# Performance work log

Measured on AMD Instinct MI355X. Metric: run time of the kernel, lower is better.

Reference implementation:

```python
import jax, jax.numpy as jnp
import numpy as np

EPS = 1e-6
HH = 4  # nheads


def _ln(x, g, b):
    mu = jnp.mean(x, axis=-1, keepdims=True)
    var = jnp.mean((x - mu) ** 2, axis=-1, keepdims=True)
    return (x - mu) * jax.lax.rsqrt(var + 1e-5) * g + b


def setup_inputs() -> dict:
    key = jax.random.key(0)
    ks = jax.random.split(key, 12)
    B, T, C, H, W = 4, 32, 128, 32, 32
    Gd = 64
    s_in = 1.0 / np.sqrt(C + Gd)
    s_c = 1.0 / np.sqrt(C)
    s_f = 1.0 / np.sqrt(4 * C)
    return {
        "x": jax.random.normal(ks[0], (B, T, C, H, W), jnp.float32),
        "guidance": jax.random.normal(ks[1], (B, T, Gd), jnp.float32),
        "Wq": jax.random.uniform(ks[2], (C + Gd, C), jnp.float32, -s_in, s_in),
        "bq": jnp.zeros((C,), jnp.float32),
        "Wk": jax.random.uniform(ks[3], (C + Gd, C), jnp.float32, -s_in, s_in),
        "bk": jnp.zeros((C,), jnp.float32),
        "Wv": jax.random.uniform(ks[4], (C, C), jnp.float32, -s_c, s_c),
        "bv": jnp.zeros((C,), jnp.float32),
        "ln1_g": jnp.ones((C,), jnp.float32),
        "ln1_b": jnp.zeros((C,), jnp.float32),
        "ln2_g": jnp.ones((C,), jnp.float32),
        "ln2_b": jnp.zeros((C,), jnp.float32),
        "W1": jax.random.uniform(ks[5], (C, 4 * C), jnp.float32, -s_c, s_c),
        "b1": jnp.zeros((4 * C,), jnp.float32),
        "W2": jax.random.uniform(ks[6], (4 * C, C), jnp.float32, -s_f, s_f),
        "b2": jnp.zeros((C,), jnp.float32),
    }


def reference(x, guidance, Wq, bq, Wk, bk, Wv, bv, ln1_g, ln1_b, ln2_g, ln2_b, W1, b1, W2, b2):
    B, T, C, H, W = x.shape
    Gd = guidance.shape[-1]
    N = B * H * W
    Hd = C // HH
    # (B,T,C,H,W) -> (N,T,C)
    x_bhw = jnp.transpose(x, (0, 3, 4, 1, 2)).reshape(N, T, C)
    g = jnp.broadcast_to(guidance[:, None, None, :, :], (B, H, W, T, Gd)).reshape(N, T, Gd)
    xqk = jnp.concatenate([x_bhw, g], axis=-1)
    q = (xqk @ Wq + bq).reshape(N, T, HH, Hd)
    k = (xqk @ Wk + bk).reshape(N, T, HH, Hd)
    v = (x_bhw @ Wv + bv).reshape(N, T, HH, Hd)
    # elu feature-map linear attention (eval mode, dropout off)
    Q = jax.nn.elu(q) + 1.0
    K = jax.nn.elu(k) + 1.0
    Vn = v / T
    KV = jnp.einsum('nshd,nshv->nhdv', K, Vn)
    Z = 1.0 / (jnp.einsum('nlhd,nhd->nlh', Q, K.sum(axis=1)) + EPS)
    out = jnp.einsum('nlhd,nhdv->nlhv', Q, KV) * Z[..., None] * T
    out = out.reshape(N, T, C)
    out = out + _ln(x_bhw, ln1_g, ln1_b)
    h = _ln(out, ln2_g, ln2_b)
    h = jax.nn.gelu(h @ W1 + b1, approximate=False) @ W2 + b2
    out = out + h
    return jnp.transpose(out.reshape(B, H, W, T, C), (0, 3, 4, 1, 2))
```

## Files before the change

kernel.cpp:

```cpp
#include <hip/hip_runtime.h>
#include <hip/hip_bf16.h>
#include <math.h>

#define T_   32
#define C_   128
#define GD_  64
#define KQK_ 192
#define NH_  4
#define HD_  32
#define C4_  512
#define HW_  1024

typedef unsigned short u16;
typedef __attribute__((ext_vector_type(8))) short short8;
typedef __attribute__((ext_vector_type(4))) short short4v;
typedef __attribute__((ext_vector_type(4))) float f32x4;
typedef __attribute__((ext_vector_type(4))) unsigned short u16x4;

#define ACF_A 0
#define ACF_C 512
#define WQH 2048
#define WQL 26624
#define WKH 51200
#define WKL 75776
#define WVH 100352
#define WVL 116736
#define W1H 133120
#define W1L 198656
#define W2H 264192
#define W2L 329728
#define GSH 395264
#define GSL 403456
#define XT  411648
#define WS_NEED_BYTES (823296ull + 4096ull*8192ull*2ull)

#define AX_H  0
#define AX_L  25600
#define X2G(g) ((g)*8704)
#define HM_H  34816
#define HM_L  52224
#define KSUM  69632
#define ZDEN  70656
#define STATS 71680
#define LN2P  72704
#define POOLB 74752

__device__ __forceinline__ float b2f(u16 u) {
    unsigned int x = ((unsigned int)u) << 16;
    float f; __builtin_memcpy(&f, &x, 4); return f;
}
__device__ __forceinline__ u16 f2b(float f) {
    __hip_bfloat16 h = __float2bfloat16(f);
    u16 u; __builtin_memcpy(&u, &h, 2); return u;
}
__device__ __forceinline__ void split2(float v, u16& h, u16& l) {
    h = f2b(v); l = f2b(v - b2f(h));
}
__device__ __forceinline__ void splitfrag(const f32x4 v, short4v& h, short4v& l) {
    u16 hh[4], ll[4];
    #pragma unroll
    for (int r = 0; r < 4; ++r) { hh[r] = f2b(v[r]); ll[r] = f2b(v[r] - b2f(hh[r])); }
    h = (short4v){(short)hh[0],(short)hh[1],(short)hh[2],(short)hh[3]};
    l = (short4v){(short)ll[0],(short)ll[1],(short)ll[2],(short)ll[3]};
}

__device__ __forceinline__ f32x4 mfma16(short4v a, short4v b, f32x4 c) {
#if __has_builtin(__builtin_amdgcn_mfma_f32_16x16x16bf16_1k)
    return __builtin_amdgcn_mfma_f32_16x16x16bf16_1k(a, b, c, 0, 0, 0);
#else
    asm("v_mfma_f32_16x16x16_bf16 %0, %1, %2, %0" : "+v"(c) : "v"(a), "v"(b));
    return c;
#endif
}

#define MFMA3(acc, ah, al, bh, bl)                                          \
    acc = __builtin_amdgcn_mfma_f32_16x16x32_bf16(ah, bh, acc, 0, 0, 0);    \
    acc = __builtin_amdgcn_mfma_f32_16x16x32_bf16(ah, bl, acc, 0, 0, 0);    \
    acc = __builtin_amdgcn_mfma_f32_16x16x32_bf16(al, bh, acc, 0, 0, 0);

#define MFMA3_16(acc, ah, al, bh, bl)                                       \
    acc = mfma16(ah, bh, acc);                                              \
    acc = mfma16(ah, bl, acc);                                              \
    acc = mfma16(al, bh, acc);

__global__ void prep_weights(const float* __restrict__ Wq, const float* __restrict__ Wk,
                             const float* __restrict__ Wv, const float* __restrict__ W1,
                             const float* __restrict__ W2, const float* __restrict__ gui,
                             const float* __restrict__ g2, const float* __restrict__ be2,
                             const float* __restrict__ b1,
                             u16* __restrict__ wsp)
{
    int e = blockIdx.x * 256 + threadIdx.x;
    if (e >= 204800) {
        int n = e - 204800;
        if (n >= 512) return;
        float a = 0.f, c = 0.f;
        for (int k = 0; k < 128; ++k) {
            float w = W1[k*512 + n];
            a = fmaf(w, g2[k], a);
            c = fmaf(w, be2[k], c);
        }
        float* acf = (float*)wsp;
        acf[ACF_A + n] = a;
        acf[ACF_C + n] = c + b1[n];
        return;
    }
    if (e >= 196608) {
        int idx = e - 196608;
        float v = gui[idx];
        u16 hb = f2b(v);
        wsp[GSH + idx] = hb;
        wsp[GSL + idx] = f2b(v - b2f(hb));
        return;
    }
    const float* src; int e2, k, n, K; int oh, ol; int isW1 = 0;
    if (e < 24576)       { src = Wq; e2 = e;          k = e2 >> 7; n = e2 & 127; K = KQK_; oh = WQH; ol = WQL; }
    else if (e < 49152)  { src = Wk; e2 = e - 24576;  k = e2 >> 7; n = e2 & 127; K = KQK_; oh = WKH; ol = WKL; }
    else if (e < 65536)  { src = Wv; e2 = e - 49152;  k = e2 >> 7; n = e2 & 127; K = C_;   oh = WVH; ol = WVL; }
    else if (e < 131072) { src = W1; e2 = e - 65536;  k = e2 >> 9; n = e2 & 511; K = C_;   oh = W1H; ol = W1L; isW1 = 1; }
    else                 { src = W2; e2 = e - 131072; k = e2 >> 7; n = e2 & 127; K = C4_;  oh = W2H; ol = W2L; }
    float w = src[e2];
    if (isW1) w *= g2[k];
    u16 hb = f2b(w);
    wsp[oh + n * K + k] = hb;
    wsp[ol + n * K + k] = f2b(w - b2f(hb));
}

__global__ __launch_bounds__(256) void transpose_x(const float* __restrict__ x, u16* __restrict__ wsp)
{
    __shared__ float tile[32][65];
    int bid = blockIdx.x;
    int hq = bid & 15, cq = (bid >> 4) & 3, t = (bid >> 6) & 31, b = bid >> 11;
    int c0 = cq * 32, hw0 = hq * 64;
    int tid = threadIdx.x;
    {
        int i = tid >> 3, j8 = (tid & 7) * 8;
        const float* src = x + ((size_t)((b*32 + t)*128 + c0 + i))*1024 + hw0 + j8;
        float4 v0 = *reinterpret_cast<const float4*>(src);
        float4 v1 = *reinterpret_cast<const float4*>(src + 4);
        tile[i][j8+0]=v0.x; tile[i][j8+1]=v0.y; tile[i][j8+2]=v0.z; tile[i][j8+3]=v0.w;
        tile[i][j8+4]=v1.x; tile[i][j8+5]=v1.y; tile[i][j8+6]=v1.z; tile[i][j8+7]=v1.w;
    }
    __syncthreads();
    {
        int jj = tid >> 2, c8 = (tid & 3) * 8;
        int n = b*1024 + hw0 + jj;
        u16 hh[8], ll[8];
        #pragma unroll
        for (int ii = 0; ii < 8; ++ii) {
            float v = tile[c8 + ii][jj];
            u16 hb = f2b(v);
            hh[ii] = hb; ll[ii] = f2b(v - b2f(hb));
        }
        u16* dh = wsp + XT + (size_t)n*8192 + t*128 + c0 + c8;
        u16* dl = dh + 4096;
        *reinterpret_cast<ushort4*>(dh)     = make_ushort4(hh[0],hh[1],hh[2],hh[3]);
        *reinterpret_cast<ushort4*>(dh + 4) = make_ushort4(hh[4],hh[5],hh[6],hh[7]);
        *reinterpret_cast<ushort4*>(dl)     = make_ushort4(ll[0],ll[1],ll[2],ll[3]);
        *reinterpret_cast<ushort4*>(dl + 4) = make_ushort4(ll[4],ll[5],ll[6],ll[7]);
    }
}

__global__ __launch_bounds__(256, 2) void fused_linattn_mfma(
    const float* __restrict__ x,
    const float* __restrict__ bq, const float* __restrict__ bk, const float* __restrict__ bv,
    const float* __restrict__ g1, const float* __restrict__ be1,
    const float* __restrict__ b2,
    const u16* __restrict__ wsp, int use_xt,
    float* __restrict__ out)
{
    extern __shared__ __align__(16) char pool[];
    float* ksum  = (float*)(pool + KSUM);
    float* zf    = (float*)(pool + ZDEN);
    float* stats = (float*)(pool + STATS);
    float* ln2p  = (float*)(pool + LN2P);
    const float* acf = (const float*)wsp;

    const int bi  = blockIdx.x;
    const int j_  = ((bi & 7) << 8) | (bi >> 3);
    const int n0  = j_ * 2;
    const int b   = n0 >> 10;
    const int hw0 = n0 & 1023;
    const int tid = threadIdx.x;
    const int lane = tid & 63, wv = tid >> 6;
    const int l16  = lane & 15, quad = lane >> 4;

    short8 wqh[6][2], wql[6][2];
    #pragma unroll
    for (int ks = 0; ks < 6; ++ks)
        #pragma unroll
        for (int nt = 0; nt < 2; ++nt) {
            const int n = (wv*2 + nt)*16 + l16;
            wqh[ks][nt] = *(const short8*)(wsp + WQH + n*KQK_ + ks*32 + quad*8);
            wql[ks][nt] = *(const short8*)(wsp + WQL + n*KQK_ + ks*32 + quad*8);
        }

    if (use_xt) {
        #pragma unroll
        for (int tau = 0; tau < 2; ++tau) {
            const u16* xtb = wsp + XT + (size_t)(n0 + tau) * 8192;
            #pragma unroll
            for (int i = 0; i < 2; ++i) {
                int off = (tid + i*256) * 8;
                int t = off >> 7, c = off & 127;
                short8 vh = *reinterpret_cast<const short8*>(xtb + off);
                short8 vl = *reinterpret_cast<const short8*>(xtb + 4096 + off);
                *reinterpret_cast<short8*>(pool + AX_H + (tau*32 + t)*400 + c*2) = vh;
                *reinterpret_cast<short8*>(pool + AX_L + (tau*32 + t)*400 + c*2) = vl;
            }
        }
    } else {
        #pragma unroll
        for (int tau = 0; tau < 2; ++tau) {
            const float* xb = x + (size_t)b * (T_*C_*HW_) + hw0 + tau;
            #pragma unroll
            for (int i = 0; i < 16; ++i) {
                int idx = tid + i*256;
                float v = xb[(size_t)idx * HW_];
                int t = idx >> 7, c = idx & 127;
                u16 hb = f2b(v);
                *(u16*)(pool + AX_H + (tau*32 + t)*400 + c*2) = hb;
                *(u16*)(pool + AX_L + (tau*32 + t)*400 + c*2) = f2b(v - b2f(hb));
            }
        }
    }
    {
        const u16* gh = wsp + GSH + b*2048 + tid*8;
        const u16* gl = wsp + GSL + b*2048 + tid*8;
        int off = tid * 8;
        int t = off >> 6, jg = off & 63;
        short8 vh = *reinterpret_cast<const short8*>(gh);
        short8 vl = *reinterpret_cast<const short8*>(gl);
        *reinterpret_cast<short8*>(pool + AX_H + t*400 + 256 + jg*2) = vh;
        *reinterpret_cast<short8*>(pool + AX_L + t*400 + 256 + jg*2) = vl;
        *reinterpret_cast<short8*>(pool + AX_H + (32 + t)*400 + 256 + jg*2) = vh;
        *reinterpret_cast<short8*>(pool + AX_L + (32 + t)*400 + 256 + jg*2) = vl;
    }
    __syncthreads();

    short4v qfh[4][2], qfl[4][2];
    short4v kfh[4][2], kfl[4][2];
    short4v vfh[4][2], vfl[4][2];

    {
        f32x4 aq[4][2];
        #pragma unroll
        for (int mt = 0; mt < 4; ++mt)
            #pragma unroll
            for (int nt = 0; nt < 2; ++nt) aq[mt][nt] = (f32x4){0.f,0.f,0.f,0.f};
        #pragma unroll
        for (int ks = 0; ks < 6; ++ks) {
            short8 ah[4], al[4];
            #pragma unroll
            for (int mt = 0; mt < 4; ++mt) {
                ah[mt] = *(const short8*)(pool + AX_H + (mt*16 + l16)*400 + ks*64 + quad*16);
                al[mt] = *(const short8*)(pool + AX_L + (mt*16 + l16)*400 + ks*64 + quad*16);
            }
            #pragma unroll
            for (int nt = 0; nt < 2; ++nt)
                #pragma unroll
                for (int mt = 0; mt < 4; ++mt) { MFMA3(aq[mt][nt], wqh[ks][nt], wql[ks][nt], ah[mt], al[mt]); }
        }
        #pragma unroll
        for (int ct = 0; ct < 2; ++ct) {
            f32x4 bq4 = *(const f32x4*)(bq + wv*32 + ct*16 + quad*4);
            #pragma unroll
            for (int mt = 0; mt < 4; ++mt) {
                f32x4 qp;
                #pragma unroll
                for (int r = 0; r < 4; ++r) {
                    float q = aq[mt][ct][r] + bq4[r];
                    qp[r] = (q > 0.f) ? q + 1.f : __expf(q);
                }
                splitfrag(qp, qfh[mt][ct], qfl[mt][ct]);
            }
        }
    }

    {
        f32x4 ak[4][2];
        #pragma unroll
        for (int mt = 0; mt < 4; ++mt)
            #pragma unroll
            for (int nt = 0; nt < 2; ++nt) ak[mt][nt] = (f32x4){0.f,0.f,0.f,0.f};
        #pragma unroll
        for (int ks = 0; ks < 6; ++ks) {
            short8 ah[4], al[4];
            #pragma unroll
            for (int mt = 0; mt < 4; ++mt) {
                ah[mt] = *(const short8*)(pool + AX_H + (mt*16 + l16)*400 + ks*64 + quad*16);
                al[mt] = *(const short8*)(pool + AX_L + (mt*16 + l16)*400 + ks*64 + quad*16);
            }
            #pragma unroll
            for (int nt = 0; nt < 2; ++nt) {
                const int n = (wv*2 + nt)*16 + l16;
                short8 bh = *(const short8*)(wsp + WKH + n*KQK_ + ks*32 + quad*8);
                short8 bl = *(const short8*)(wsp + WKL + n*KQK_ + ks*32 + quad*8);
                #pragma unroll
                for (int mt = 0; mt < 4; ++mt) { MFMA3(ak[mt][nt], ah[mt], al[mt], bh, bl); }
            }
        }
        float sk[2][2] = {{0.f,0.f},{0.f,0.f}};
        #pragma unroll
        for (int nt = 0; nt < 2; ++nt) {
            float bias = bk[wv*32 + nt*16 + l16];
            #pragma unroll
            for (int mt = 0; mt < 4; ++mt) {
                f32x4 kp;
                #pragma unroll
                for (int r = 0; r < 4; ++r) {
                    float k = ak[mt][nt][r] + bias;
                    float v = (k > 0.f) ? k + 1.f : __expf(k);
                    kp[r] = v;
                    sk[mt >> 1][nt] += v;
                }
                splitfrag(kp, kfh[mt][nt], kfl[mt][nt]);
            }
        }
        #pragma unroll
        for (int tau = 0; tau < 2; ++tau)
            #pragma unroll
            for (int nt = 0; nt < 2; ++nt) {
                float s = sk[tau][nt];
                s += __shfl_xor(s, 16); s += __shfl_xor(s, 32);
                if (quad == 0) ksum[tau*128 + wv*32 + nt*16 + l16] = s;
            }
    }

    {
        f32x4 av[4][2];
        #pragma unroll
        for (int mt = 0; mt < 4; ++mt)
            #pragma unroll
            for (int nt = 0; nt < 2; ++nt) av[mt][nt] = (f32x4){0.f,0.f,0.f,0.f};
        #pragma unroll
        for (int ks = 0; ks < 4; ++ks) {
            short8 ah[4], al[4];
            #pragma unroll
            for (int mt = 0; mt < 4; ++mt) {
                ah[mt] = *(const short8*)(pool + AX_H + (mt*16 + l16)*400 + ks*64 + quad*16);
                al[mt] = *(const short8*)(pool + AX_L + (mt*16 + l16)*400 + ks*64 + quad*16);
            }
            #pragma unroll
            for (int nt = 0; nt < 2; ++nt) {
                const int n = (wv*2 + nt)*16 + l16;
                short8 bh = *(const short8*)(wsp + WVH + n*C_ + ks*32 + quad*8);
                short8 bl = *(const short8*)(wsp + WVL + n*C_ + ks*32 + quad*8);
                #pragma unroll
                for (int mt = 0; mt < 4; ++mt) { MFMA3(av[mt][nt], ah[mt], al[mt], bh, bl); }
            }
        }
        #pragma unroll
        for (int nt = 0; nt < 2; ++nt) {
            float bias = bv[wv*32 + nt*16 + l16];
            #pragma unroll
            for (int mt = 0; mt < 4; ++mt) {
                f32x4 vp;
                #pragma unroll
                for (int r = 0; r < 4; ++r) vp[r] = av[mt][nt][r] + bias;
                splitfrag(vp, vfh[mt][nt], vfl[mt][nt]);
            }
        }
    }

    #pragma unroll
    for (int tau = 0; tau < 2; ++tau) {
        f32x4 ka0 = *(const f32x4*)(ksum + tau*128 + wv*32 + quad*4);
        f32x4 ka1 = *(const f32x4*)(ksum + tau*128 + wv*32 + 16 + quad*4);
        #pragma unroll
        for (int lt = 0; lt < 2; ++lt) {
            const int mt = tau*2 + lt;
            float p = 0.f;
            #pragma unroll
            for (int i = 0; i < 4; ++i) {
                p = fmaf(b2f((u16)(short)qfh[mt][0][i]) + b2f((u16)(short)qfl[mt][0][i]), ka0[i], p);
                p = fmaf(b2f((u16)(short)qfh[mt][1][i]) + b2f((u16)(short)qfl[mt][1][i]), ka1[i], p);
            }
            p += __shfl_xor(p, 16); p += __shfl_xor(p, 32);
            if (quad == 0) zf[tau*128 + wv*32 + lt*16 + l16] = 1.f / (p + 1e-6f);
        }
    }

    short4v kvfh[2][2][2], kvfl[2][2][2];
    #pragma unroll
    for (int tau = 0; tau < 2; ++tau)
        #pragma unroll
        for (int dt = 0; dt < 2; ++dt)
            #pragma unroll
            for (int vt = 0; vt < 2; ++vt) {
                f32x4 kv = (f32x4){0.f,0.f,0.f,0.f};
                #pragma unroll
                for (int lt = 0; lt < 2; ++lt) {
                    const int mt = tau*2 + lt;
                    MFMA3_16(kv, kfh[mt][dt], kfl[mt][dt], vfh[mt][vt], vfl[mt][vt]);
                }
                splitfrag(kv, kvfh[tau][dt][vt], kvfl[tau][dt][vt]);
            }

    {
        int t = tid >> 2, jj = tid & 3;
        const char* rp = pool + AX_H + t*400 + jj*64;
        float m = 0.f, s = 0.f;
        #pragma unroll
        for (int p8 = 0; p8 < 4; ++p8) {
            short8 h = *(const short8*)(rp + p8*16);
            short8 l = *(const short8*)(rp + (AX_L - AX_H) + p8*16);
            #pragma unroll
            for (int i = 0; i < 8; ++i) {
                float v = b2f((u16)h[i]) + b2f((u16)l[i]);
                m += v; s = fmaf(v, v, s);
            }
        }
        m += __shfl_xor(m, 1); s += __shfl_xor(s, 1);
        m += __shfl_xor(m, 2); s += __shfl_xor(s, 2);
        if (jj == 0) {
            float mu = m * (1.f/C_);
            stats[t]      = mu;
            stats[64 + t] = rsqrtf(s * (1.f/C_) - mu*mu + 1e-5f);
        }
    }
    __syncthreads();

    f32x4 o1v[4][2];
    #pragma unroll
    for (int mt = 0; mt < 4; ++mt) {
        const int tau = mt >> 1;
        f32x4 zd4 = *(const f32x4*)(zf + tau*128 + wv*32 + (mt & 1)*16 + quad*4);
        f32x4 mu4 = *(const f32x4*)(stats + mt*16 + quad*4);
        f32x4 rs4 = *(const f32x4*)(stats + 64 + mt*16 + quad*4);
        #pragma unroll
        for (int vt = 0; vt < 2; ++vt) {
            f32x4 oa = (f32x4){0.f,0.f,0.f,0.f};
            #pragma unroll
            for (int dt = 0; dt < 2; ++dt) {
                MFMA3_16(oa, qfh[mt][dt], qfl[mt][dt], kvfh[tau][dt][vt], kvfl[tau][dt][vt]);
            }
            int ch = wv*32 + vt*16 + l16;
            float g1c = g1[ch], be1c = be1[ch];
            #pragma unroll
            for (int r = 0; r < 4; ++r) {
                int row = mt*16 + quad*4 + r;
                float xv = b2f(*(const u16*)(pool + AX_H + row*400 + ch*2))
                         + b2f(*(const u16*)(pool + AX_L + row*400 + ch*2));
                o1v[mt][vt][r] = oa[r]*zd4[r] + (xv - mu4[r])*rs4[r]*g1c + be1c;
            }
        }
    }
    {
        #pragma unroll
        for (int mt = 0; mt < 4; ++mt)
            #pragma unroll
            for (int r = 0; r < 4; ++r) {
                float v0 = o1v[mt][0][r], v1 = o1v[mt][1][r];
                float m = v0 + v1;
                float s = v0*v0 + v1*v1;
                m += __shfl_xor(m, 1); s += __shfl_xor(s, 1);
                m += __shfl_xor(m, 2); s += __shfl_xor(s, 2);
                m += __shfl_xor(m, 4); s += __shfl_xor(s, 4);
                m += __shfl_xor(m, 8); s += __shfl_xor(s, 8);
                if (l16 == 0) {
                    int row = mt*16 + quad*4 + r;
                    ln2p[wv*64 + row]       = m;
                    ln2p[256 + wv*64 + row] = s;
                }
            }
    }
    __syncthreads();

    #pragma unroll
    for (int mt = 0; mt < 4; ++mt) {
        char* xb = pool + X2G(mt);
        #pragma unroll
        for (int vt = 0; vt < 2; ++vt) {
            int ch = wv*32 + vt*16 + l16;
            #pragma unroll
            for (int r = 0; r < 4; ++r) {
                u16 hb, lb; split2(o1v[mt][vt][r], hb, lb);
                int off = (quad*4 + r)*272 + ch*2;
                *(u16*)(xb + off)        = hb;
                *(u16*)(xb + 4352 + off) = lb;
            }
        }
    }
    if (tid < 64) {
        int t = tid;
        float m = 0.f, s = 0.f;
        #pragma unroll
        for (int w = 0; w < 4; ++w) { m += ln2p[w*64 + t]; s += ln2p[256 + w*64 + t]; }
        float mu = m * (1.f/C_);
        float rs = rsqrtf(s * (1.f/C_) - mu*mu + 1e-5f);
        stats[128 + t] = mu * rs;
        stats[192 + t] = rs;
    }
    __syncthreads();

    f32x4 accO[4][2];
    #pragma unroll
    for (int mt = 0; mt < 4; ++mt)
        #pragma unroll
        for (int nt = 0; nt < 2; ++nt) accO[mt][nt] = (f32x4){0.f,0.f,0.f,0.f};

    #pragma unroll 1
    for (int mh = 0; mh < 4; ++mh) {
        {
            f32x4 accH[4][2];
            #pragma unroll
            for (int mt = 0; mt < 4; ++mt)
                #pragma unroll
                for (int nt = 0; nt < 2; ++nt) accH[mt][nt] = (f32x4){0.f,0.f,0.f,0.f};
            #pragma unroll
            for (int ks = 0; ks < 4; ++ks) {
                short8 ah[4], al[4];
                #pragma unroll
                for (int mt = 0; mt < 4; ++mt) {
                    const char* xb = pool + X2G(mt) + l16*272 + ks*64 + quad*16;
                    ah[mt] = *(const short8*)(xb);
                    al[mt] = *(const short8*)(xb + 4352);
                }
                #pragma unroll
                for (int nt = 0; nt < 2; ++nt) {
                    const int gn = mh*128 + (wv*2 + nt)*16 + l16;
                    short8 bh = *(const short8*)(wsp + W1H + gn*C_ + ks*32 + quad*8);
                    short8 bl = *(const short8*)(wsp + W1L + gn*C_ + ks*32 + quad*8);
                    #pragma unroll
                    for (int mt = 0; mt < 4; ++mt) { MFMA3(accH[mt][nt], bh, bl, ah[mt], al[mt]); }
                }
            }
            #pragma unroll
            for (int nt = 0; nt < 2; ++nt) {
                int base = mh*128 + (wv*2 + nt)*16 + quad*4;
                f32x4 a4 = *(const f32x4*)(acf + ACF_A + base);
                f32x4 c4 = *(const f32x4*)(acf + ACF_C + base);
                int ch0 = (wv*2 + nt)*16 + quad*4;
                #pragma unroll
                for (int mt = 0; mt < 4; ++mt) {
                    int tk = mt*16 + l16;
                    float mrs = stats[128 + tk], rsv = stats[192 + tk];
                    u16 hh[4], ll[4];
                    #pragma unroll
                    for (int r = 0; r < 4; ++r) {
                        float v = accH[mt][nt][r]*rsv - mrs*a4[r] + c4[r];
                        float ge = 0.5f * v * (1.f + erff(v * 0.70710678118654752f));
                        split2(ge, hh[r], ll[r]);
                    }
                    char* hb = pool + HM_H + tk*272 + ch0*2;
                    *(u16x4*)(hb)                    = (u16x4){hh[0],hh[1],hh[2],hh[3]};
                    *(u16x4*)(hb + (HM_L - HM_H))    = (u16x4){ll[0],ll[1],ll[2],ll[3]};
                }
            }
        }
        __syncthreads();
        {
            #pragma unroll
            for (int ks = 0; ks < 4; ++ks) {
                short8 ah[4], al[4];
                #pragma unroll
                for (int mt = 0; mt < 4; ++mt) {
                    const char* hb = pool + HM_H + (mt*16 + l16)*272 + ks*64 + quad*16;
                    ah[mt] = *(const short8*)(hb);
                    al[mt] = *(const short8*)(hb + (HM_L - HM_H));
                }
                #pragma unroll
                for (int nt = 0; nt < 2; ++nt) {
                    const int n = (wv*2 + nt)*16 + l16;
                    short8 bh = *(const short8*)(wsp + W2H + n*C4_ + mh*128 + ks*32 + quad*8);
                    short8 bl = *(const short8*)(wsp + W2L + n*C4_ + mh*128 + ks*32 + quad*8);
                    #pragma unroll
                    for (int mt = 0; mt < 4; ++mt) { MFMA3(accO[mt][nt], ah[mt], al[mt], bh, bl); }
                }
            }
        }
        if (mh < 3) __syncthreads();
    }

    {
        float* obase = out + (size_t)b * (T_*C_*HW_) + hw0;
        #pragma unroll
        for (int mt = 0; mt < 4; ++mt) {
            const int tau = mt >> 1;
            float* ob = obase + tau;
            #pragma unroll
            for (int nt = 0; nt < 2; ++nt) {
                int ch = wv*32 + nt*16 + l16;
                float b2c = b2[ch];
                #pragma unroll
                for (int r = 0; r < 4; ++r) {
                    int t = (mt & 1)*16 + quad*4 + r;
                    float y = o1v[mt][nt][r] + accO[mt][nt][r] + b2c;
                    ob[(size_t)(t*C_ + ch) * HW_] = y;
                }
            }
        }
    }
}

extern "C" void kernel_launch(void* const* d_in, const int* in_sizes, int n_in,
                              void* d_out, int out_size, void* d_ws, size_t ws_size,
                              hipStream_t stream)
{
    const float* x   = (const float*)d_in[0];
    const float* gui = (const float*)d_in[1];
    const float* Wq  = (const float*)d_in[2];
    const float* bq  = (const float*)d_in[3];
    const float* Wk  = (const float*)d_in[4];
    const float* bk  = (const float*)d_in[5];
    const float* Wv  = (const float*)d_in[6];
    const float* bv  = (const float*)d_in[7];
    const float* g1  = (const float*)d_in[8];
    const float* be1 = (const float*)d_in[9];
    const float* g2  = (const float*)d_in[10];
    const float* be2 = (const float*)d_in[11];
    const float* W1  = (const float*)d_in[12];
    const float* b1  = (const float*)d_in[13];
    const float* W2  = (const float*)d_in[14];
    const float* b2  = (const float*)d_in[15];
    u16* wsp = (u16*)d_ws;

    int use_xt = (ws_size >= WS_NEED_BYTES) ? 1 : 0;

    prep_weights<<<dim3(802), dim3(256), 0, stream>>>(Wq, Wk, Wv, W1, W2, gui, g2, be2, b1, wsp);
    if (use_xt)
        transpose_x<<<dim3(8192), dim3(256), 0, stream>>>(x, wsp);

    (void)hipFuncSetAttribute((const void*)fused_linattn_mfma,
                              hipFuncAttributeMaxDynamicSharedMemorySize,
                              POOLB);
    fused_linattn_mfma<<<dim3(2048), dim3(256), POOLB, stream>>>(
        x, bq, bk, bv, g1, be1, b2, wsp, use_xt, (float*)d_out);
}
```

Before: 450.9 us.

## Shrink LDS footprint with XOR-swizzled layout to fit three blocks per CU

Replaces padded LDS rows with XOR-swizzled 256-byte rows to avoid bank conflicts without padding. Stores guidance once (32 rows) instead of duplicating it per pixel, and reuses the activation buffer for the FFN input. The FFN hidden tile is processed in two halves of 32 rows so it needs less scratch LDS. Together these cut LDS from about 74KB to 54KB and raise launch bounds from 2 to 3 blocks per CU. The cost is extra barriers per FFN chunk and tighter register budgets, which could cause spills.

Measured after the change: 775.9 us. +72.1%, slower.

```diff
diff --git a/kernel.cpp b/kernel.cpp
--- a/kernel.cpp
+++ b/kernel.cpp
@@ -34,16 +34,20 @@
 #define XT  411648
 #define WS_NEED_BYTES (823296ull + 4096ull*8192ull*2ull)
 
-#define AX_H  0
-#define AX_L  25600
-#define X2G(g) ((g)*8704)
-#define HM_H  34816
-#define HM_L  52224
-#define KSUM  69632
-#define ZDEN  70656
-#define STATS 71680
-#define LN2P  72704
-#define POOLB 74752
+#define AXH 0
+#define AXL 16384
+#define GH  32768
+#define GL  36864
+#define HMH 32768
+#define HML 40960
+#define KSUM  49152
+#define ZDEN  50176
+#define STATS 51200
+#define LN2P  52224
+#define POOLB 54272
+
+#define AXB(row, colb)  ((row)*256 + (((colb) ^ (((row)&7)<<4))))
+#define GSW(row, colb)  ((row)*128 + (((colb) ^ (((row)&7)<<4))))
 
 __device__ __forceinline__ float b2f(u16 u) {
     unsigned int x = ((unsigned int)u) << 16;
@@ -161,7 +165,7 @@
     }
 }
 
-__global__ __launch_bounds__(256, 2) void fused_linattn_mfma(
+__global__ __launch_bounds__(256, 3) void fused_linattn_mfma(
     const float* __restrict__ x,
     const float* __restrict__ bq, const float* __restrict__ bk, const float* __restrict__ bv,
     const float* __restrict__ g1, const float* __restrict__ be1,
@@ -203,10 +207,11 @@
             for (int i = 0; i < 2; ++i) {
                 int off = (tid + i*256) * 8;
                 int t = off >> 7, c = off & 127;
+                int grow = tau*32 + t;
                 short8 vh = *reinterpret_cast<const short8*>(xtb + off);
                 short8 vl = *reinterpret_cast<const short8*>(xtb + 4096 + off);
-                *reinterpret_cast<short8*>(pool + AX_H + (tau*32 + t)*400 + c*2) = vh;
-                *reinterpret_cast<short8*>(pool + AX_L + (tau*32 + t)*400 + c*2) = vl;
+                *reinterpret_cast<short8*>(pool + AXH + AXB(grow, c*2)) = vh;
+                *reinterpret_cast<short8*>(pool + AXL + AXB(grow, c*2)) = vl;
             }
         }
     } else {
@@ -218,23 +223,21 @@
                 int idx = tid + i*256;
                 float v = xb[(size_t)idx * HW_];
                 int t = idx >> 7, c = idx & 127;
+                int grow = tau*32 + t;
                 u16 hb = f2b(v);
-                *(u16*)(pool + AX_H + (tau*32 + t)*400 + c*2) = hb;
-                *(u16*)(pool + AX_L + (tau*32 + t)*400 + c*2) = f2b(v - b2f(hb));
+                *(u16*)(pool + AXH + AXB(grow, c*2)) = hb;
+                *(u16*)(pool + AXL + AXB(grow, c*2)) = f2b(v - b2f(hb));
             }
         }
     }
     {
         const u16* gh = wsp + GSH + b*2048 + tid*8;
         const u16* gl = wsp + GSL + b*2048 + tid*8;
-        int off = tid * 8;
-        int t = off >> 6, jg = off & 63;
+        int t = tid >> 3, jg = (tid & 7) * 8;
         short8 vh = *reinterpret_cast<const short8*>(gh);
         short8 vl = *reinterpret_cast<const short8*>(gl);
-        *reinterpret_cast<short8*>(pool + AX_H + t*400 + 256 + jg*2) = vh;
-        *reinterpret_cast<short8*>(pool + AX_L + t*400 + 256 + jg*2) = vl;
-        *reinterpret_cast<short8*>(pool + AX_H + (32 + t)*400 + 256 + jg*2) = vh;
-        *reinterpret_cast<short8*>(pool + AX_L + (32 + t)*400 + 256 + jg*2) = vl;
+        *reinterpret_cast<short8*>(pool + GH + GSW(t, jg*2)) = vh;
+        *reinterpret_cast<short8*>(pool + GL + GSW(t, jg*2)) = vl;
     }
     __syncthreads();
 
@@ -251,10 +254,21 @@
         #pragma unroll
         for (int ks = 0; ks < 6; ++ks) {
             short8 ah[4], al[4];
-            #pragma unroll
-            for (int mt = 0; mt < 4; ++mt) {
-                ah[mt] = *(const short8*)(pool + AX_H + (mt*16 + l16)*400 + ks*64 + quad*16);
-                al[mt] = *(const short8*)(pool + AX_L + (mt*16 + l16)*400 + ks*64 + quad*16);
+            if (ks < 4) {
+                #pragma unroll
+                for (int mt = 0; mt < 4; ++mt) {
+                    ah[mt] = *(const short8*)(pool + AXH + AXB(mt*16 + l16, ks*64 + quad*16));
+                    al[mt] = *(const short8*)(pool + AXL + AXB(mt*16 + l16, ks*64 + quad*16));
+                }
+            } else {
+                #pragma unroll
+                for (int mh2 = 0; mh2 < 2; ++mh2) {
+                    int trow = mh2*16 + l16;
+                    short8 gh2 = *(const short8*)(pool + GH + GSW(trow, (ks-4)*64 + quad*16));
+                    short8 gl2 = *(const short8*)(pool + GL + GSW(trow, (ks-4)*64 + quad*16));
+                    ah[mh2] = gh2; ah[mh2+2] = gh2;
+                    al[mh2] = gl2; al[mh2+2] = gl2;
+                }
             }
             #pragma unroll
             for (int nt = 0; nt < 2; ++nt)
@@ -286,10 +300,21 @@
         #pragma unroll
         for (int ks = 0; ks < 6; ++ks) {
             short8 ah[4], al[4];
-            #pragma unroll
-            for (int mt = 0; mt < 4; ++mt) {
-                ah[mt] = *(const short8*)(pool + AX_H + (mt*16 + l16)*400 + ks*64 + quad*16);
-                al[mt] = *(const short8*)(pool + AX_L + (mt*16 + l16)*400 + ks*64 + quad*16);
+            if (ks < 4) {
+                #pragma unroll
+                for (int mt = 0; mt < 4; ++mt) {
+                    ah[mt] = *(const short8*)(pool + AXH + AXB(mt*16 + l16, ks*64 + quad*16));
+                    al[mt] = *(const short8*)(pool + AXL + AXB(mt*16 + l16, ks*64 + quad*16));
+                }
+            } else {
+                #pragma unroll
+                for (int mh2 = 0; mh2 < 2; ++mh2) {
+                    int trow = mh2*16 + l16;
+                    short8 gh2 = *(const short8*)(pool + GH + GSW(trow, (ks-4)*64 + quad*16));
+                    short8 gl2 = *(const short8*)(pool + GL + GSW(trow, (ks-4)*64 + quad*16));
+                    ah[mh2] = gh2; ah[mh2+2] = gh2;
+                    al[mh2] = gl2; al[mh2+2] = gl2;
+                }
             }
             #pragma unroll
             for (int nt = 0; nt < 2; ++nt) {
@@ -338,8 +363,8 @@
             short8 ah[4], al[4];
             #pragma unroll
             for (int mt = 0; mt < 4; ++mt) {
-                ah[mt] = *(const short8*)(pool + AX_H + (mt*16 + l16)*400 + ks*64 + quad*16);
-                al[mt] = *(const short8*)(pool + AX_L + (mt*16 + l16)*400 + ks*64 + quad*16);
+                ah[mt] = *(const short8*)(pool + AXH + AXB(mt*16 + l16, ks*64 + quad*16));
+                al[mt] = *(const short8*)(pool + AXL + AXB(mt*16 + l16, ks*64 + quad*16));
             }
             #pragma unroll
             for (int nt = 0; nt < 2; ++nt) {
@@ -399,12 +424,12 @@
 
     {
         int t = tid >> 2, jj = tid & 3;
-        const char* rp = pool + AX_H + t*400 + jj*64;
         float m = 0.f, s = 0.f;
         #pragma unroll
         for (int p8 = 0; p8 < 4; ++p8) {
-            short8 h = *(const short8*)(rp + p8*16);
-            short8 l = *(const short8*)(rp + (AX_L - AX_H) + p8*16);
+            int colb = jj*64 + p8*16;
+            short8 h = *(const short8*)(pool + AXH + AXB(t, colb));
+            short8 l = *(const short8*)(pool + AXL + AXB(t, colb));
             #pragma unroll
             for (int i = 0; i < 8; ++i) {
                 float v = b2f((u16)h[i]) + b2f((u16)l[i]);
@@ -440,8 +465,8 @@
             #pragma unroll
             for (int r = 0; r < 4; ++r) {
                 int row = mt*16 + quad*4 + r;
-                float xv = b2f(*(const u16*)(pool + AX_H + row*400 + ch*2))
-                         + b2f(*(const u16*)(pool + AX_L + row*400 + ch*2));
+                float xv = b2f(*(const u16*)(pool + AXH + AXB(row, ch*2)))
+                         + b2f(*(const u16*)(pool + AXL + AXB(row, ch*2)));
                 o1v[mt][vt][r] = oa[r]*zd4[r] + (xv - mu4[r])*rs4[r]*g1c + be1c;
             }
         }
@@ -469,16 +494,15 @@
 
     #pragma unroll
     for (int mt = 0; mt < 4; ++mt) {
-        char* xb = pool + X2G(mt);
         #pragma unroll
         for (int vt = 0; vt < 2; ++vt) {
             int ch = wv*32 + vt*16 + l16;
             #pragma unroll
             for (int r = 0; r < 4; ++r) {
+                int row = mt*16 + quad*4 + r;
                 u16 hb, lb; split2(o1v[mt][vt][r], hb, lb);
-                int off = (quad*4 + r)*272 + ch*2;
-                *(u16*)(xb + off)        = hb;
-                *(u16*)(xb + 4352 + off) = lb;
+                *(u16*)(pool + AXH + AXB(row, ch*2)) = hb;
+                *(u16*)(pool + AXL + AXB(row, ch*2)) = lb;
             }
         }
     }
@@ -502,75 +526,78 @@
 
     #pragma unroll 1
     for (int mh = 0; mh < 4; ++mh) {
-        {
-            f32x4 accH[4][2];
-            #pragma unroll
-            for (int mt = 0; mt < 4; ++mt)
-                #pragma unroll
-                for (int nt = 0; nt < 2; ++nt) accH[mt][nt] = (f32x4){0.f,0.f,0.f,0.f};
-            #pragma unroll
-            for (int ks = 0; ks < 4; ++ks) {
-                short8 ah[4], al[4];
-                #pragma unroll
-                for (int mt = 0; mt < 4; ++mt) {
-                    const char* xb = pool + X2G(mt) + l16*272 + ks*64 + quad*16;
-                    ah[mt] = *(const short8*)(xb);
-                    al[mt] = *(const short8*)(xb + 4352);
+        #pragma unroll 1
+        for (int half = 0; half < 2; ++half) {
+            {
+                f32x4 accH[2][2];
+                #pragma unroll
+                for (int mtl = 0; mtl < 2; ++mtl)
+                    #pragma unroll
+                    for (int nt = 0; nt < 2; ++nt) accH[mtl][nt] = (f32x4){0.f,0.f,0.f,0.f};
+                #pragma unroll
+                for (int ks = 0; ks < 4; ++ks) {
+                    short8 ah[2], al[2];
+                    #pragma unroll
+                    for (int mtl = 0; mtl < 2; ++mtl) {
+                        int row = (half*2 + mtl)*16 + l16;
+                        ah[mtl] = *(const short8*)(pool + AXH + AXB(row, ks*64 + quad*16));
+                        al[mtl] = *(const short8*)(pool + AXL + AXB(row, ks*64 + quad*16));
+                    }
+                    #pragma unroll
+                    for (int nt = 0; nt < 2; ++nt) {
+                        const int gn = mh*128 + (wv*2 + nt)*16 + l16;
+                        short8 bh = *(const short8*)(wsp + W1H + gn*C_ + ks*32 + quad*8);
+                        short8 bl = *(const short8*)(wsp + W1L + gn*C_ + ks*32 + quad*8);
+                        #pragma unroll
+                        for (int mtl = 0; mtl < 2; ++mtl) { MFMA3(accH[mtl][nt], bh, bl, ah[mtl], al[mtl]); }
+                    }
                 }
                 #pragma unroll
                 for (int nt = 0; nt < 2; ++nt) {
-                    const int gn = mh*128 + (wv*2 + nt)*16 + l16;
-                    short8 bh = *(const short8*)(wsp + W1H + gn*C_ + ks*32 + quad*8);
-                    short8 bl = *(const short8*)(wsp + W1L + gn*C_ + ks*32 + quad*8);
+                    int base = mh*128 + (wv*2 + nt)*16 + quad*4;
+                    f32x4 a4 = *(const f32x4*)(acf + ACF_A + base);
+                    f32x4 c4 = *(const f32x4*)(acf + ACF_C + base);
+                    int ch0 = (wv*2 + nt)*16 + quad*4;
                     #pragma unroll
-                    for (int mt = 0; mt < 4; ++mt) { MFMA3(accH[mt][nt], bh, bl, ah[mt], al[mt]); }
-                }
-            }
-            #pragma unroll
-            for (int nt = 0; nt < 2; ++nt) {
-                int base = mh*128 + (wv*2 + nt)*16 + quad*4;
-                f32x4 a4 = *(const f32x4*)(acf + ACF_A + base);
-                f32x4 c4 = *(const f32x4*)(acf + ACF_C + base);
-                int ch0 = (wv*2 + nt)*16 + quad*4;
-                #pragma unroll
-                for (int mt = 0; mt < 4; ++mt) {
-                    int tk = mt*16 + l16;
-                    float mrs = stats[128 + tk], rsv = stats[192 + tk];
-                    u16 hh[4], ll[4];
+                    for (int mtl = 0; mtl < 2; ++mtl) {
+                        int tk = mtl*16 + l16;
+                        int tkg = half*32 + tk;
+                        float mrs = stats[128 + tkg], rsv = stats[192 + tkg];
+                        u16 hh[4], ll[4];
+                        #pragma unroll
+                        for (int r = 0; r < 4; ++r) {
+                            float v = accH[mtl][nt][r]*rsv - mrs*a4[r] + c4[r];
+                            float ge = 0.5f * v * (1.f + erff(v * 0.70710678118654752f));
+                            split2(ge, hh[r], ll[r]);
+                        }
+                        *(u16x4*)(pool + HMH + AXB(tk, ch0*2)) = (u16x4){hh[0],hh[1],hh[2],hh[3]};
+                        *(u16x4*)(pool + HML + AXB(tk, ch0*2)) = (u16x4){ll[0],ll[1],ll[2],ll[3]};
+                    }
+                }
+            }
+            __syncthreads();
+            {
+                #pragma unroll
+                for (int ks = 0; ks < 4; ++ks) {
+                    short8 ah[2], al[2];
                     #pragma unroll
-                    for (int r = 0; r < 4; ++r) {
-                        float v = accH[mt][nt][r]*rsv - mrs*a4[r] + c4[r];
-                        float ge = 0.5f * v * (1.f + erff(v * 0.70710678118654752f));
-                        split2(ge, hh[r], ll[r]);
+                    for (int mtl = 0; mtl < 2; ++mtl) {
+                        int row = mtl*16 + l16;
+                        ah[mtl] = *(const short8*)(pool + HMH + AXB(row, ks*64 + quad*16));
+                        al[mtl] = *(const short8*)(pool + HML + AXB(row, ks*64 + quad*16));
                     }
-                    char* hb = pool + HM_H + tk*272 + ch0*2;
-                    *(u16x4*)(hb)                    = (u16x4){hh[0],hh[1],hh[2],hh[3]};
-                    *(u16x4*)(hb + (HM_L - HM_H))    = (u16x4){ll[0],ll[1],ll[2],ll[3]};
-                }
-            }
-        }
-        __syncthreads();
-        {
-            #pragma unroll
-            for (int ks = 0; ks < 4; ++ks) {
-                short8 ah[4], al[4];
-                #pragma unroll
-                for (int mt = 0; mt < 4; ++mt) {
-                    const char* hb = pool + HM_H + (mt*16 + l16)*272 + ks*64 + quad*16;
-                    ah[mt] = *(const short8*)(hb);
-                    al[mt] = *(const short8*)(hb + (HM_L - HM_H));
-                }
-                #pragma unroll
-                for (int nt = 0; nt < 2; ++nt) {
-                    const int n = (wv*2 + nt)*16 + l16;
-                    short8 bh = *(const short8*)(wsp + W2H + n*C4_ + mh*128 + ks*32 + quad*8);
-                    short8 bl = *(const short8*)(wsp + W2L + n*C4_ + mh*128 + ks*32 + quad*8);
                     #pragma unroll
-                    for (int mt = 0; mt < 4; ++mt) { MFMA3(accO[mt][nt], ah[mt], al[mt], bh, bl); }
-                }
-            }
-        }
-        if (mh < 3) __syncthreads();
+                    for (int nt = 0; nt < 2; ++nt) {
+                        const int n = (wv*2 + nt)*16 + l16;
+                        short8 bh = *(const short8*)(wsp + W2H + n*C4_ + mh*128 + ks*32 + quad*8);
+                        short8 bl = *(const short8*)(wsp + W2L + n*C4_ + mh*128 + ks*32 + quad*8);
+                        #pragma unroll
+                        for (int mtl = 0; mtl < 2; ++mtl) { MFMA3(accO[half*2 + mtl][nt], ah[mtl], al[mtl], bh, bl); }
+                    }
+                }
+            }
+            if (!(mh == 3 && half == 1)) __syncthreads();
+        }
     }
 
     {
```

## Software-prefetch weight fragments into registers ahead of each MFMA stage

Applied to the files above, without the earlier changes.

Weight fragments for K, V, W1 and W2 are now loaded from global memory into register arrays one stage early, during the preceding matmul or epilogue, instead of inside the MFMA inner loops. The W1 slice for the next hidden chunk is prefetched after the W2 pass of the current chunk. The aim is to hide global-load latency behind compute, at the cost of many extra live VGPRs, which may lower occupancy or cause spills.

Result: slower. 485.6 us (+7.7%).

```diff
diff --git a/kernel.cpp b/kernel.cpp
--- a/kernel.cpp
+++ b/kernel.cpp
@@ -241,6 +241,8 @@
     short4v qfh[4][2], qfl[4][2];
     short4v kfh[4][2], kfl[4][2];
     short4v vfh[4][2], vfl[4][2];
+    short8 wkh[6][2], wkl[6][2];
+    short8 wvh[4][2], wvl[4][2];
 
     {
         f32x4 aq[4][2];
@@ -262,6 +264,14 @@
                 for (int mt = 0; mt < 4; ++mt) { MFMA3(aq[mt][nt], wqh[ks][nt], wql[ks][nt], ah[mt], al[mt]); }
         }
         #pragma unroll
+        for (int ks = 0; ks < 6; ++ks)
+            #pragma unroll
+            for (int nt = 0; nt < 2; ++nt) {
+                const int n = (wv*2 + nt)*16 + l16;
+                wkh[ks][nt] = *(const short8*)(wsp + WKH + n*KQK_ + ks*32 + quad*8);
+                wkl[ks][nt] = *(const short8*)(wsp + WKL + n*KQK_ + ks*32 + quad*8);
+            }
+        #pragma unroll
         for (int ct = 0; ct < 2; ++ct) {
             f32x4 bq4 = *(const f32x4*)(bq + wv*32 + ct*16 + quad*4);
             #pragma unroll
@@ -292,14 +302,18 @@
                 al[mt] = *(const short8*)(pool + AX_L + (mt*16 + l16)*400 + ks*64 + quad*16);
             }
             #pragma unroll
+            for (int nt = 0; nt < 2; ++nt)
+                #pragma unroll
+                for (int mt = 0; mt < 4; ++mt) { MFMA3(ak[mt][nt], ah[mt], al[mt], wkh[ks][nt], wkl[ks][nt]); }
+        }
+        #pragma unroll
+        for (int ks = 0; ks < 4; ++ks)
+            #pragma unroll
             for (int nt = 0; nt < 2; ++nt) {
                 const int n = (wv*2 + nt)*16 + l16;
-                short8 bh = *(const short8*)(wsp + WKH + n*KQK_ + ks*32 + quad*8);
-                short8 bl = *(const short8*)(wsp + WKL + n*KQK_ + ks*32 + quad*8);
-                #pragma unroll
-                for (int mt = 0; mt < 4; ++mt) { MFMA3(ak[mt][nt], ah[mt], al[mt], bh, bl); }
-            }
-        }
+                wvh[ks][nt] = *(const short8*)(wsp + WVH + n*C_ + ks*32 + quad*8);
+                wvl[ks][nt] = *(const short8*)(wsp + WVL + n*C_ + ks*32 + quad*8);
+            }
         float sk[2][2] = {{0.f,0.f},{0.f,0.f}};
         #pragma unroll
         for (int nt = 0; nt < 2; ++nt) {
@@ -342,13 +356,9 @@
                 al[mt] = *(const short8*)(pool + AX_L + (mt*16 + l16)*400 + ks*64 + quad*16);
             }
             #pragma unroll
-            for (int nt = 0; nt < 2; ++nt) {
-                const int n = (wv*2 + nt)*16 + l16;
-                short8 bh = *(const short8*)(wsp + WVH + n*C_ + ks*32 + quad*8);
-                short8 bl = *(const short8*)(wsp + WVL + n*C_ + ks*32 + quad*8);
-                #pragma unroll
-                for (int mt = 0; mt < 4; ++mt) { MFMA3(av[mt][nt], ah[mt], al[mt], bh, bl); }
-            }
+            for (int nt = 0; nt < 2; ++nt)
+                #pragma unroll
+                for (int mt = 0; mt < 4; ++mt) { MFMA3(av[mt][nt], ah[mt], al[mt], wvh[ks][nt], wvl[ks][nt]); }
         }
         #pragma unroll
         for (int nt = 0; nt < 2; ++nt) {
@@ -467,6 +477,15 @@
     }
     __syncthreads();
 
+    short8 w1h[4][2], w1l[4][2], w2h[4][2], w2l[4][2];
+    #pragma unroll
+    for (int ks = 0; ks < 4; ++ks)
+        #pragma unroll
+        for (int nt = 0; nt < 2; ++nt) {
+            const int gn = (wv*2 + nt)*16 + l16;
+            w1h[ks][nt] = *(const short8*)(wsp + W1H + gn*C_ + ks*32 + quad*8);
+            w1l[ks][nt] = *(const short8*)(wsp + W1L + gn*C_ + ks*32 + quad*8);
+        }
     #pragma unroll
     for (int mt = 0; mt < 4; ++mt) {
         char* xb = pool + X2G(mt);
@@ -518,14 +537,18 @@
                     al[mt] = *(const short8*)(xb + 4352);
                 }
                 #pragma unroll
+                for (int nt = 0; nt < 2; ++nt)
+                    #pragma unroll
+                    for (int mt = 0; mt < 4; ++mt) { MFMA3(accH[mt][nt], w1h[ks][nt], w1l[ks][nt], ah[mt], al[mt]); }
+            }
+            #pragma unroll
+            for (int ks = 0; ks < 4; ++ks)
+                #pragma unroll
                 for (int nt = 0; nt < 2; ++nt) {
-                    const int gn = mh*128 + (wv*2 + nt)*16 + l16;
-                    short8 bh = *(const short8*)(wsp + W1H + gn*C_ + ks*32 + quad*8);
-                    short8 bl = *(const short8*)(wsp + W1L + gn*C_ + ks*32 + quad*8);
-                    #pragma unroll
-                    for (int mt = 0; mt < 4; ++mt) { MFMA3(accH[mt][nt], bh, bl, ah[mt], al[mt]); }
-                }
-            }
+                    const int n = (wv*2 + nt)*16 + l16;
+                    w2h[ks][nt] = *(const short8*)(wsp + W2H + n*C4_ + mh*128 + ks*32 + quad*8);
+                    w2l[ks][nt] = *(const short8*)(wsp + W2L + n*C4_ + mh*128 + ks*32 + quad*8);
+                }
             #pragma unroll
             for (int nt = 0; nt < 2; ++nt) {
                 int base = mh*128 + (wv*2 + nt)*16 + quad*4;
@@ -561,13 +584,19 @@
                     al[mt] = *(const short8*)(hb + (HM_L - HM_H));
                 }
                 #pragma unroll
-                for (int nt = 0; nt < 2; ++nt) {
-                    const int n = (wv*2 + nt)*16 + l16;
-                    short8 bh = *(const short8*)(wsp + W2H + n*C4_ + mh*128 + ks*32 + quad*8);
-                    short8 bl = *(const short8*)(wsp + W2L + n*C4_ + mh*128 + ks*32 + quad*8);
+                for (int nt = 0; nt < 2; ++nt)
                     #pragma unroll
-                    for (int mt = 0; mt < 4; ++mt) { MFMA3(accO[mt][nt], ah[mt], al[mt], bh, bl); }
-                }
+                    for (int mt = 0; mt < 4; ++mt) { MFMA3(accO[mt][nt], ah[mt], al[mt], w2h[ks][nt], w2l[ks][nt]); }
+            }
+            if (mh < 3) {
+                #pragma unroll
+                for (int ks = 0; ks < 4; ++ks)
+                    #pragma unroll
+                    for (int nt = 0; nt < 2; ++nt) {
+                        const int gn = (mh+1)*128 + (wv*2 + nt)*16 + l16;
+                        w1h[ks][nt] = *(const short8*)(wsp + W1H + gn*C_ + ks*32 + quad*8);
+                        w1l[ks][nt] = *(const short8*)(wsp + W1L + gn*C_ + ks*32 + quad*8);
+                    }
             }
         }
         if (mh < 3) __syncthreads();
```
